# Kernel optimization log

Measured on AMD Instinct MI355X. Metric: run time of the kernel, lower is better.

## Reference

```python
import jax, jax.numpy as jnp
import numpy as np
from jax import lax

B, T, D = 2048, 300, 40
H = 64          # BasicLSTMCell num_units
D1 = 128        # dense1 units
OUT = 512       # out_dim (num speakers)
FORGET_BIAS = 1.0
BN_EPS = 1e-3   # tf.layers.BatchNormalization default


def setup_inputs() -> dict:
    key = jax.random.key(0)
    ks = jax.random.split(key, 10)
    X = jax.random.normal(ks[0], (B, T, D), dtype=jnp.float32)
    seq_length = jax.random.randint(ks[1], (B,), 1, T + 1).astype(jnp.int32)
    # BasicLSTMCell kernel: [input_dim + H, 4H], gate order i, j, f, o
    lstm_kernel = jax.random.normal(ks[2], (D + H, 4 * H), dtype=jnp.float32) * 0.08
    lstm_bias = jnp.zeros((4 * H,), dtype=jnp.float32)
    W1 = jax.random.normal(ks[3], (H, D1), dtype=jnp.float32) * 0.1
    b1 = jnp.zeros((D1,), dtype=jnp.float32)
    gamma = jnp.ones((D1,), dtype=jnp.float32)
    beta = jnp.zeros((D1,), dtype=jnp.float32)
    moving_mean = jnp.zeros((D1,), dtype=jnp.float32)
    moving_var = jnp.ones((D1,), dtype=jnp.float32)
    W2 = jax.random.normal(ks[4], (D1, OUT), dtype=jnp.float32) * 0.1
    b2 = jnp.zeros((OUT,), dtype=jnp.float32)
    return {"X": X, "seq_length": seq_length,
            "lstm_kernel": lstm_kernel, "lstm_bias": lstm_bias,
            "W1": W1, "b1": b1, "gamma": gamma, "beta": beta,
            "moving_mean": moving_mean, "moving_var": moving_var,
            "W2": W2, "b2": b2}


def reference(X, seq_length, lstm_kernel, lstm_bias, W1, b1, gamma, beta,
              moving_mean, moving_var, W2, b2):
    b = X.shape[0]
    c0 = jnp.zeros((b, H), dtype=X.dtype)
    h0 = jnp.zeros((b, H), dtype=X.dtype)

    def step(carry, x_t):
        c, h = carry
        z = jnp.concatenate([x_t, h], axis=1) @ lstm_kernel + lstm_bias
        i, j, f, o = jnp.split(z, 4, axis=1)
        new_c = c * jax.nn.sigmoid(f + FORGET_BIAS) + jax.nn.sigmoid(i) * jnp.tanh(j)
        new_h = jnp.tanh(new_c) * jax.nn.sigmoid(o)
        return (new_c, new_h), new_h

    _, outs = lax.scan(step, (c0, h0), jnp.swapaxes(X, 0, 1))  # [T, B, H]
    outs = jnp.swapaxes(outs, 0, 1)  # [B, T, H]

    # gather last valid timestep per sample
    idx = (seq_length - 1).astype(jnp.int32)
    final = jnp.take_along_axis(outs, idx[:, None, None], axis=1)[:, 0, :]  # [B, H]

    x = jax.nn.relu(final @ W1 + b1)
    # BatchNorm in inference mode (training=False): use moving statistics
    x = gamma * (x - moving_mean) * lax.rsqrt(moving_var + BN_EPS) + beta
    return jax.nn.softmax(x @ W2 + b2, axis=-1)
```

## Files before the change

### kernel.cpp

```cpp
#include <hip/hip_runtime.h>
#include <stdint.h>

#define TT 300
#define DD 40
#define SB 8
#define AROW 200
#define ZROW 260

typedef __attribute__((ext_vector_type(8))) short short8;
typedef __attribute__((ext_vector_type(4))) float f32x4;

__device__ __forceinline__ ushort f2bf(float f) {
  uint32_t b = __float_as_uint(f);
  b += 0x7FFFu + ((b >> 16) & 1u);
  return (ushort)(b >> 16);
}
__device__ __forceinline__ float sigm(float x) {
  return __builtin_amdgcn_rcpf(1.0f + __expf(-x));
}
__device__ __forceinline__ float tanh_f(float x) {
  return 1.0f - 2.0f * __builtin_amdgcn_rcpf(1.0f + __expf(2.0f * x));
}

__global__ __launch_bounds__(256, 1) void lstm_mfma_kernel(
    const float* __restrict__ X, const int* __restrict__ seqlen,
    const float* __restrict__ Wk, const float* __restrict__ bias,
    float* __restrict__ hfin)
{
  __shared__ ushort wstage[64 * 128];
  __shared__ ushort Ash[16 * AROW];
  __shared__ float zbuf[8 * ZROW];

  const int tid = threadIdx.x;
  const int wv = tid >> 6, lane = tid & 63;
  const int s0 = blockIdx.x * SB;

  for (int i = tid; i < 16 * AROW; i += 256) Ash[i] = 0;

  short8 Bf[6][4];
  for (int c = 0; c < 4; ++c) {
    __syncthreads();
    for (int i = tid; i < 64 * 128; i += 256) {
      int kp = i >> 6, cc = i & 63;
      ushort v = 0;
      int ks = (kp < 40) ? kp : ((kp >= 64) ? (kp - 24) : -1);
      if (ks >= 0) {
        int u = c * 16 + (cc >> 2), g = cc & 3;
        v = f2bf(Wk[ks * 256 + g * 64 + u]);
      }
      wstage[cc * 128 + kp] = v;
    }
    __syncthreads();
    if (wv == c) {
      #pragma unroll
      for (int kt = 0; kt < 6; ++kt) {
        int kk = ((kt < 4) ? kt * 32 : (kt * 32 - 64)) + (lane >> 4) * 8;
        #pragma unroll
        for (int nt = 0; nt < 4; ++nt) {
          int cc = nt * 16 + (lane & 15);
          Bf[kt][nt] = *reinterpret_cast<const short8*>(&wstage[cc * 128 + kk]);
        }
      }
    }
  }

  const int ps = tid >> 5;
  const int u0 = (2 * tid) & 63, u1 = u0 + 1;
  const int mylen = seqlen[s0 + ps];
  const float bi0 = bias[u0],      bj0 = bias[64 + u0];
  const float bfg0 = bias[128 + u0] + 1.0f, bo0 = bias[192 + u0];
  const float bi1 = bias[u1],      bj1 = bias[64 + u1];
  const float bfg1 = bias[128 + u1] + 1.0f, bo1 = bias[192 + u1];

  int ml = seqlen[s0 + (lane & 7)];
  #pragma unroll
  for (int off = 1; off < 64; off <<= 1) ml = max(ml, __shfl_xor(ml, off));

  const int iA = tid, iB = 256 + tid;
  const int sA = (iA * 205) >> 13, dA = iA - sA * 40;
  int sB = (iB * 205) >> 13; if (sB > 7) sB = 7;
  const int dB = iB - sB * 40;
  const float* xpA = X + (size_t)(s0 + sA) * (TT * DD) + dA;
  const float* xpB = X + (size_t)(s0 + sB) * (TT * DD) + dB;
  const bool hasB = (iB < SB * DD);

  Ash[sA * AROW + dA] = f2bf(xpA[0]);
  if (hasB) Ash[sB * AROW + dB] = f2bf(xpB[0]);
  __syncthreads();

  float c0 = 0.f, c1 = 0.f, hf0 = 0.f, hf1 = 0.f;

  for (int t = 0; t < ml; ++t) {
    short8 Af[6];
    #pragma unroll
    for (int kt = 0; kt < 6; ++kt)
      Af[kt] = *reinterpret_cast<const short8*>(
          &Ash[(lane & 15) * AROW + kt * 32 + (lane >> 4) * 8]);

    const bool pre = (t + 1 < ml);
    float xnA = 0.f, xnB = 0.f;
    if (pre) {
      xnA = xpA[(t + 1) * DD];
      if (hasB) xnB = xpB[(t + 1) * DD];
    }

    f32x4 zero4 = {0.f, 0.f, 0.f, 0.f};
    f32x4 acc[4] = {zero4, zero4, zero4, zero4};
    #pragma unroll
    for (int kt = 0; kt < 6; ++kt) {
      #pragma unroll
      for (int nt = 0; nt < 4; ++nt)
        acc[nt] = __builtin_amdgcn_mfma_f32_16x16x32_bf16(Af[kt], Bf[kt][nt], acc[nt], 0, 0, 0);
    }

    if (lane < 32) {
      const int q = lane >> 4, cl = lane & 15;
      #pragma unroll
      for (int nt = 0; nt < 4; ++nt) {
        #pragma unroll
        for (int r = 0; r < 4; ++r)
          zbuf[(q * 4 + r) * ZROW + wv * 64 + nt * 16 + cl] = acc[nt][r];
      }
    }
    __syncthreads();

    f32x4 z0 = *reinterpret_cast<const f32x4*>(&zbuf[ps * ZROW + u0 * 4]);
    f32x4 z1 = *reinterpret_cast<const f32x4*>(&zbuf[ps * ZROW + u1 * 4]);
    float nc0 = c0 * sigm(z0[2] + bfg0) + sigm(z0[0] + bi0) * tanh_f(z0[1] + bj0);
    float nh0 = tanh_f(nc0) * sigm(z0[3] + bo0);
    float nc1 = c1 * sigm(z1[2] + bfg1) + sigm(z1[0] + bi1) * tanh_f(z1[1] + bj1);
    float nh1 = tanh_f(nc1) * sigm(z1[3] + bo1);
    c0 = nc0; c1 = nc1;
    if (t == mylen - 1) { hf0 = nh0; hf1 = nh1; }

    ushort hh0 = f2bf(nh0);
    ushort hl0 = f2bf(nh0 - __uint_as_float((uint32_t)hh0 << 16));
    ushort hh1 = f2bf(nh1);
    ushort hl1 = f2bf(nh1 - __uint_as_float((uint32_t)hh1 << 16));
    Ash[ps * AROW + 64 + u0] = hh0;
    Ash[ps * AROW + 128 + u0] = hl0;
    Ash[ps * AROW + 64 + u1] = hh1;
    Ash[ps * AROW + 128 + u1] = hl1;
    if (pre) {
      Ash[sA * AROW + dA] = f2bf(xnA);
      if (hasB) Ash[sB * AROW + dB] = f2bf(xnB);
    }
    __syncthreads();
  }

  hfin[(size_t)(s0 + ps) * 64 + u0] = hf0;
  hfin[(size_t)(s0 + ps) * 64 + u1] = hf1;
}

__global__ __launch_bounds__(256, 1) void head_kernel(
    const float* __restrict__ hfin,
    const float* __restrict__ W1, const float* __restrict__ b1,
    const float* __restrict__ gamma, const float* __restrict__ beta,
    const float* __restrict__ mmean, const float* __restrict__ mvar,
    const float* __restrict__ W2, const float* __restrict__ b2,
    float* __restrict__ out)
{
  __shared__ float hl[16 * 64];
  __shared__ float d1t[128 * 20];
  __shared__ float lg[16 * 516];
  const int tid = threadIdx.x;
  const int b0 = blockIdx.x * 16;

  for (int i = tid; i < 16 * 64; i += 256) hl[i] = hfin[(size_t)b0 * 64 + i];
  __syncthreads();

  {
    const int j = tid & 127, sg = tid >> 7;
    float acc[8];
    const float bb = b1[j];
    #pragma unroll
    for (int s = 0; s < 8; ++s) acc[s] = bb;
    for (int k = 0; k < 64; ++k) {
      float w = W1[k * 128 + j];
      #pragma unroll
      for (int s = 0; s < 8; ++s) acc[s] = fmaf(hl[(sg * 8 + s) * 64 + k], w, acc[s]);
    }
    const float ga = gamma[j], be = beta[j], mm = mmean[j];
    const float iv = rsqrtf(mvar[j] + 1e-3f);
    #pragma unroll
    for (int s = 0; s < 8; ++s) {
      float v = fmaxf(acc[s], 0.f);
      d1t[j * 20 + sg * 8 + s] = ga * (v - mm) * iv + be;
    }
  }
  __syncthreads();

  {
    const int cA = tid * 2;
    float accA[16], accB[16];
    const float bA = b2[cA], bB = b2[cA + 1];
    #pragma unroll
    for (int s = 0; s < 16; ++s) { accA[s] = bA; accB[s] = bB; }
    for (int k = 0; k < 128; ++k) {
      const float2 w = *reinterpret_cast<const float2*>(&W2[k * 512 + cA]);
      const f32x4 dq0 = *reinterpret_cast<const f32x4*>(&d1t[k * 20]);
      const f32x4 dq1 = *reinterpret_cast<const f32x4*>(&d1t[k * 20 + 4]);
      const f32x4 dq2 = *reinterpret_cast<const f32x4*>(&d1t[k * 20 + 8]);
      const f32x4 dq3 = *reinterpret_cast<const f32x4*>(&d1t[k * 20 + 12]);
      #pragma unroll
      for (int s = 0; s < 4; ++s) {
        accA[s]      = fmaf(dq0[s], w.x, accA[s]);      accB[s]      = fmaf(dq0[s], w.y, accB[s]);
        accA[s + 4]  = fmaf(dq1[s], w.x, accA[s + 4]);  accB[s + 4]  = fmaf(dq1[s], w.y, accB[s + 4]);
        accA[s + 8]  = fmaf(dq2[s], w.x, accA[s + 8]);  accB[s + 8]  = fmaf(dq2[s], w.y, accB[s + 8]);
        accA[s + 12] = fmaf(dq3[s], w.x, accA[s + 12]); accB[s + 12] = fmaf(dq3[s], w.y, accB[s + 12]);
      }
    }
    #pragma unroll
    for (int s = 0; s < 16; ++s) {
      lg[s * 516 + cA]     = accA[s];
      lg[s * 516 + cA + 1] = accB[s];
    }
  }
  __syncthreads();

  {
    const int w = tid >> 6, lane = tid & 63;
    #pragma unroll
    for (int si = 0; si < 4; ++si) {
      const int s = w * 4 + si;
      float v[8];
      float m = -3.4e38f;
      #pragma unroll
      for (int i = 0; i < 8; ++i) { v[i] = lg[s * 516 + lane + 64 * i]; m = fmaxf(m, v[i]); }
      #pragma unroll
      for (int off = 1; off < 64; off <<= 1) m = fmaxf(m, __shfl_xor(m, off));
      float sum = 0.f;
      #pragma unroll
      for (int i = 0; i < 8; ++i) { v[i] = __expf(v[i] - m); sum += v[i]; }
      #pragma unroll
      for (int off = 1; off < 64; off <<= 1) sum += __shfl_xor(sum, off);
      const float inv = __builtin_amdgcn_rcpf(sum);
      #pragma unroll
      for (int i = 0; i < 8; ++i)
        out[(size_t)(b0 + s) * 512 + lane + 64 * i] = v[i] * inv;
    }
  }
}

extern "C" void kernel_launch(void* const* d_in, const int* in_sizes, int n_in,
                              void* d_out, int out_size, void* d_ws, size_t ws_size,
                              hipStream_t stream) {
  const float* X      = (const float*)d_in[0];
  const int*   seqlen = (const int*)d_in[1];
  const float* Wk     = (const float*)d_in[2];
  const float* bias   = (const float*)d_in[3];
  const float* W1     = (const float*)d_in[4];
  const float* b1     = (const float*)d_in[5];
  const float* gam    = (const float*)d_in[6];
  const float* bet    = (const float*)d_in[7];
  const float* mmean  = (const float*)d_in[8];
  const float* mvar   = (const float*)d_in[9];
  const float* W2     = (const float*)d_in[10];
  const float* b2     = (const float*)d_in[11];
  float* out  = (float*)d_out;
  float* hfin = (float*)d_ws;

  lstm_mfma_kernel<<<dim3(256), dim3(256), 0, stream>>>(X, seqlen, Wk, bias, hfin);
  head_kernel<<<dim3(128), dim3(256), 0, stream>>>(hfin, W1, b1, gam, bet,
                                                   mmean, mvar, W2, b2, out);
}
```

Measured before the change: 428.1 us.

## Compute LSTM gates in MFMA registers and double-buffer A tile

```diff
diff --git a/kernel.cpp b/kernel.cpp
--- a/kernel.cpp
+++ b/kernel.cpp
@@ -5,7 +5,7 @@
 #define DD 40
 #define SB 8
 #define AROW 200
-#define ZROW 260
+#define ABUF (16 * AROW)
 
 typedef __attribute__((ext_vector_type(8))) short short8;
 typedef __attribute__((ext_vector_type(4))) float f32x4;
@@ -14,12 +14,6 @@
   uint32_t b = __float_as_uint(f);
   b += 0x7FFFu + ((b >> 16) & 1u);
   return (ushort)(b >> 16);
-}
-__device__ __forceinline__ float sigm(float x) {
-  return __builtin_amdgcn_rcpf(1.0f + __expf(-x));
-}
-__device__ __forceinline__ float tanh_f(float x) {
-  return 1.0f - 2.0f * __builtin_amdgcn_rcpf(1.0f + __expf(2.0f * x));
 }
 
 __global__ __launch_bounds__(256, 1) void lstm_mfma_kernel(
@@ -27,129 +21,138 @@
     const float* __restrict__ Wk, const float* __restrict__ bias,
     float* __restrict__ hfin)
 {
-  __shared__ ushort wstage[64 * 128];
-  __shared__ ushort Ash[16 * AROW];
-  __shared__ float zbuf[8 * ZROW];
+  __shared__ ushort wstage[64 * 192];
+  __shared__ ushort Ash[2 * ABUF];
 
   const int tid = threadIdx.x;
   const int wv = tid >> 6, lane = tid & 63;
   const int s0 = blockIdx.x * SB;
 
-  for (int i = tid; i < 16 * AROW; i += 256) Ash[i] = 0;
+  for (int i = tid; i < 2 * ABUF; i += 256) Ash[i] = 0;
 
   short8 Bf[6][4];
   for (int c = 0; c < 4; ++c) {
     __syncthreads();
-    for (int i = tid; i < 64 * 128; i += 256) {
-      int kp = i >> 6, cc = i & 63;
+    for (int i = tid; i < 64 * 192; i += 256) {
+      int cc = i & 63, kp = i >> 6;
+      int g = cc >> 4, u = c * 16 + (cc & 15);
+      int col = g * 64 + u;
       ushort v = 0;
-      int ks = (kp < 40) ? kp : ((kp >= 64) ? (kp - 24) : -1);
-      if (ks >= 0) {
-        int u = c * 16 + (cc >> 2), g = cc & 3;
-        v = f2bf(Wk[ks * 256 + g * 64 + u]);
+      if (kp < 40) {
+        v = f2bf(Wk[kp * 256 + col]);
+      } else if (kp < 42) {
+        float bv = bias[col] + ((g == 2) ? 1.0f : 0.0f);
+        ushort hi = f2bf(bv);
+        v = (kp == 40) ? hi : f2bf(bv - __uint_as_float((uint32_t)hi << 16));
+      } else if (kp >= 64) {
+        v = f2bf(Wk[(40 + ((kp - 64) >> 1)) * 256 + col]);
       }
-      wstage[cc * 128 + kp] = v;
+      wstage[cc * 192 + kp] = v;
     }
     __syncthreads();
     if (wv == c) {
       #pragma unroll
       for (int kt = 0; kt < 6; ++kt) {
-        int kk = ((kt < 4) ? kt * 32 : (kt * 32 - 64)) + (lane >> 4) * 8;
+        int kk = kt * 32 + (lane >> 4) * 8;
         #pragma unroll
-        for (int nt = 0; nt < 4; ++nt) {
-          int cc = nt * 16 + (lane & 15);
-          Bf[kt][nt] = *reinterpret_cast<const short8*>(&wstage[cc * 128 + kk]);
-        }
+        for (int g = 0; g < 4; ++g)
+          Bf[kt][g] = *reinterpret_cast<const short8*>(
+              &wstage[(g * 16 + (lane & 15)) * 192 + kk]);
       }
     }
   }
 
-  const int ps = tid >> 5;
-  const int u0 = (2 * tid) & 63, u1 = u0 + 1;
-  const int mylen = seqlen[s0 + ps];
-  const float bi0 = bias[u0],      bj0 = bias[64 + u0];
-  const float bfg0 = bias[128 + u0] + 1.0f, bo0 = bias[192 + u0];
-  const float bi1 = bias[u1],      bj1 = bias[64 + u1];
-  const float bfg1 = bias[128 + u1] + 1.0f, bo1 = bias[192 + u1];
+  const int u = wv * 16 + (lane & 15);
+  const int q = lane >> 4;
+  const int sl0 = 2 * q, sl1 = sl0 + 1;
+  const int len0 = seqlen[s0 + sl0], len1 = seqlen[s0 + sl1];
 
   int ml = seqlen[s0 + (lane & 7)];
   #pragma unroll
-  for (int off = 1; off < 64; off <<= 1) ml = max(ml, __shfl_xor(ml, off));
+  for (int off = 1; off < 8; off <<= 1) ml = max(ml, __shfl_xor(ml, off));
 
   const int iA = tid, iB = 256 + tid;
   const int sA = (iA * 205) >> 13, dA = iA - sA * 40;
   int sB = (iB * 205) >> 13; if (sB > 7) sB = 7;
   const int dB = iB - sB * 40;
-  const float* xpA = X + (size_t)(s0 + sA) * (TT * DD) + dA;
-  const float* xpB = X + (size_t)(s0 + sB) * (TT * DD) + dB;
+  const int rA = 4 * (sA >> 1) + (sA & 1), rB = 4 * (sB >> 1) + (sB & 1);
+  const float* pA = X + (size_t)(s0 + sA) * (TT * DD) + dA;
+  const float* pB = X + (size_t)(s0 + sB) * (TT * DD) + dB;
   const bool hasB = (iB < SB * DD);
-
-  Ash[sA * AROW + dA] = f2bf(xpA[0]);
-  if (hasB) Ash[sB * AROW + dB] = f2bf(xpB[0]);
-  __syncthreads();
+  const int xiA = rA * AROW + dA, xiB = rB * AROW + dB;
+
+  if (tid < 16) {
+    int s = tid & 7, b = tid >> 3;
+    int row = 4 * (s >> 1) + (s & 1);
+    Ash[b * ABUF + row * AROW + 40] = 0x3F80;
+    Ash[b * ABUF + row * AROW + 41] = 0x3F80;
+  }
+  Ash[xiA] = f2bf(pA[0]);
+  if (hasB) Ash[xiB] = f2bf(pB[0]);
+  __syncthreads();
+  pA += DD; pB += DD;
 
   float c0 = 0.f, c1 = 0.f, hf0 = 0.f, hf1 = 0.f;
+  int rb = 0, wb = ABUF;
+  const int afb = (lane & 15) * AROW + q * 8;
+  const int hw0 = (q * 4) * AROW + 64 + 2 * u;
+  const int hw1 = (q * 4 + 1) * AROW + 64 + 2 * u;
 
   for (int t = 0; t < ml; ++t) {
     short8 Af[6];
     #pragma unroll
     for (int kt = 0; kt < 6; ++kt)
-      Af[kt] = *reinterpret_cast<const short8*>(
-          &Ash[(lane & 15) * AROW + kt * 32 + (lane >> 4) * 8]);
+      Af[kt] = *reinterpret_cast<const short8*>(&Ash[rb + afb + kt * 32]);
 
     const bool pre = (t + 1 < ml);
     float xnA = 0.f, xnB = 0.f;
     if (pre) {
-      xnA = xpA[(t + 1) * DD];
-      if (hasB) xnB = xpB[(t + 1) * DD];
+      xnA = pA[0]; pA += DD;
+      if (hasB) { xnB = pB[0]; pB += DD; }
     }
 
     f32x4 zero4 = {0.f, 0.f, 0.f, 0.f};
-    f32x4 acc[4] = {zero4, zero4, zero4, zero4};
+    f32x4 acc0 = zero4, acc1 = zero4, acc2 = zero4, acc3 = zero4;
     #pragma unroll
     for (int kt = 0; kt < 6; ++kt) {
-      #pragma unroll
-      for (int nt = 0; nt < 4; ++nt)
-        acc[nt] = __builtin_amdgcn_mfma_f32_16x16x32_bf16(Af[kt], Bf[kt][nt], acc[nt], 0, 0, 0);
-    }
-
-    if (lane < 32) {
-      const int q = lane >> 4, cl = lane & 15;
-      #pragma unroll
-      for (int nt = 0; nt < 4; ++nt) {
-        #pragma unroll
-        for (int r = 0; r < 4; ++r)
-          zbuf[(q * 4 + r) * ZROW + wv * 64 + nt * 16 + cl] = acc[nt][r];
-      }
-    }
-    __syncthreads();
-
-    f32x4 z0 = *reinterpret_cast<const f32x4*>(&zbuf[ps * ZROW + u0 * 4]);
-    f32x4 z1 = *reinterpret_cast<const f32x4*>(&zbuf[ps * ZROW + u1 * 4]);
-    float nc0 = c0 * sigm(z0[2] + bfg0) + sigm(z0[0] + bi0) * tanh_f(z0[1] + bj0);
-    float nh0 = tanh_f(nc0) * sigm(z0[3] + bo0);
-    float nc1 = c1 * sigm(z1[2] + bfg1) + sigm(z1[0] + bi1) * tanh_f(z1[1] + bj1);
-    float nh1 = tanh_f(nc1) * sigm(z1[3] + bo1);
+      acc0 = __builtin_amdgcn_mfma_f32_16x16x32_bf16(Af[kt], Bf[kt][0], acc0, 0, 0, 0);
+      acc1 = __builtin_amdgcn_mfma_f32_16x16x32_bf16(Af[kt], Bf[kt][1], acc1, 0, 0, 0);
+      acc2 = __builtin_amdgcn_mfma_f32_16x16x32_bf16(Af[kt], Bf[kt][2], acc2, 0, 0, 0);
+      acc3 = __builtin_amdgcn_mfma_f32_16x16x32_bf16(Af[kt], Bf[kt][3], acc3, 0, 0, 0);
+    }
+
+    float Ef0 = __expf(-acc2[0]), Ei0 = __expf(-acc0[0]), Ej0 = __expf(2.f * acc1[0]);
+    float nc0 = fmaf(c0, __builtin_amdgcn_rcpf(1.f + Ef0),
+                     (Ej0 - 1.f) * __builtin_amdgcn_rcpf((1.f + Ei0) * (1.f + Ej0)));
+    float En0 = __expf(2.f * fminf(nc0, 44.f)), Eo0 = __expf(-acc3[0]);
+    float nh0 = (En0 - 1.f) * __builtin_amdgcn_rcpf((1.f + En0) * (1.f + Eo0));
+
+    float Ef1 = __expf(-acc2[1]), Ei1 = __expf(-acc0[1]), Ej1 = __expf(2.f * acc1[1]);
+    float nc1 = fmaf(c1, __builtin_amdgcn_rcpf(1.f + Ef1),
+                     (Ej1 - 1.f) * __builtin_amdgcn_rcpf((1.f + Ei1) * (1.f + Ej1)));
+    float En1 = __expf(2.f * fminf(nc1, 44.f)), Eo1 = __expf(-acc3[1]);
+    float nh1 = (En1 - 1.f) * __builtin_amdgcn_rcpf((1.f + En1) * (1.f + Eo1));
+
     c0 = nc0; c1 = nc1;
-    if (t == mylen - 1) { hf0 = nh0; hf1 = nh1; }
+    if (t == len0 - 1) hf0 = nh0;
+    if (t == len1 - 1) hf1 = nh1;
 
     ushort hh0 = f2bf(nh0);
     ushort hl0 = f2bf(nh0 - __uint_as_float((uint32_t)hh0 << 16));
     ushort hh1 = f2bf(nh1);
     ushort hl1 = f2bf(nh1 - __uint_as_float((uint32_t)hh1 << 16));
-    Ash[ps * AROW + 64 + u0] = hh0;
-    Ash[ps * AROW + 128 + u0] = hl0;
-    Ash[ps * AROW + 64 + u1] = hh1;
-    Ash[ps * AROW + 128 + u1] = hl1;
+    *reinterpret_cast<uint32_t*>(&Ash[wb + hw0]) = (uint32_t)hh0 | ((uint32_t)hl0 << 16);
+    *reinterpret_cast<uint32_t*>(&Ash[wb + hw1]) = (uint32_t)hh1 | ((uint32_t)hl1 << 16);
     if (pre) {
-      Ash[sA * AROW + dA] = f2bf(xnA);
-      if (hasB) Ash[sB * AROW + dB] = f2bf(xnB);
+      Ash[wb + xiA] = f2bf(xnA);
+      if (hasB) Ash[wb + xiB] = f2bf(xnB);
     }
     __syncthreads();
-  }
-
-  hfin[(size_t)(s0 + ps) * 64 + u0] = hf0;
-  hfin[(size_t)(s0 + ps) * 64 + u1] = hf1;
+    rb ^= ABUF; wb ^= ABUF;
+  }
+
+  hfin[(size_t)(s0 + sl0) * 64 + u] = hf0;
+  hfin[(size_t)(s0 + sl1) * 64 + u] = hf1;
 }
 
 __global__ __launch_bounds__(256, 1) void head_kernel(
```

Result: faster. 407.8 us (-4.7%).
